# Optimization experiments

Hardware: AMD Instinct MI355X
Metric: run time of the kernel (lower is better)

## Reference

```python
import jax, jax.numpy as jnp
from jax import lax
import numpy as np

B, C, HH, WW = 8, 64, 128, 128
N = HH * WW
EPS = 1e-5


def _roll_h(xn, sign):
    # per-channel cyclic roll along H: out[b,c,h,w] = xn[b,c,(h - sign*c) % H, w]
    _, Cx, Hx, _ = xn.shape
    c = jnp.arange(Cx)[:, None]
    idx = (jnp.arange(Hx)[None, :] - sign * jnp.arange(Cx)[:, None]) % Hx  # (C,H)
    return xn[:, c, idx, :]


def _roll_w(xn, sign):
    return _roll_h(xn.transpose(0, 1, 3, 2), sign).transpose(0, 1, 3, 2)


def _ch_linear(xn, w, b):
    # nn.Linear over the channel dim of a BCHW tensor (token-MLP on (B,N,C))
    return jnp.einsum('bchw,cd->bdhw', xn, w) + b[None, :, None, None]


def _bn(xn, g, b):
    # BatchNorm2d, training-mode stats (biased var over B,H,W)
    m = xn.mean(axis=(0, 2, 3), keepdims=True)
    v = xn.var(axis=(0, 2, 3), keepdims=True)
    return (xn - m) * lax.rsqrt(v + EPS) * g[None, :, None, None] + b[None, :, None, None]


def _dwconv(xn, w, dil, pad):
    return lax.conv_general_dilated(xn, w, (1, 1), ((pad, pad), (pad, pad)),
                                    rhs_dilation=(dil, dil),
                                    dimension_numbers=('NCHW', 'OIHW', 'NCHW'),
                                    feature_group_count=xn.shape[1])


def _pc(xn, w):
    # 1x1 pointwise conv, no bias; w: (C_out, C_in)
    return jnp.einsum('bchw,oc->bohw', xn, w)


def lgff_forward(x, fc1_w, fc1_b, fc2_w, fc2_b, fc3_w, fc3_b, fc4_w, fc4_b,
                 fc5_w, fc5_b, ln_g, ln_b, pc_w, dw_w, dw_b, dw_bn_g, dw_bn_b,
                 dd_w, dd_bn_g, dd_bn_b, se_w1, se_b1, se_w2, se_b2, H, W):
    Bx, Nx, Cx = x.shape
    xn = x.transpose(0, 2, 1).reshape(Bx, Cx, H, W)
    # branch 1: roll+c along H -> fc1 -> GELU -> roll+c along W -> fc2
    a = jax.nn.gelu(_ch_linear(_roll_h(xn, 1), fc1_w, fc1_b), approximate=False)
    x_1 = _ch_linear(_roll_w(a, 1), fc2_w, fc2_b) + xn
    # branch 2: roll-c along W -> fc3 -> GELU -> roll+c along H -> fc4
    b = jax.nn.gelu(_ch_linear(_roll_w(xn, -1), fc3_w, fc3_b), approximate=False)
    x_2 = _ch_linear(_roll_h(b, 1), fc4_w, fc4_b) + xn
    # concat along feature dim (token layout dim=2 == channel dim here), LayerNorm(2C), fc5
    xc = jnp.concatenate([x_1, x_2], axis=1)  # (B, 2C, H, W)
    m = xc.mean(axis=1, keepdims=True)
    v = xc.var(axis=1, keepdims=True)
    xc = (xc - m) * lax.rsqrt(v + EPS) * ln_g[None, :, None, None] + ln_b[None, :, None, None]
    x1 = _ch_linear(xc, fc5_w, fc5_b) + xn
    # conv fusion part
    x2 = _pc(x1, pc_w)
    y = jax.nn.relu(_bn(_dwconv(x2, dw_w, 1, 1) + dw_b[None, :, None, None], dw_bn_g, dw_bn_b))
    y = jax.nn.relu(_bn(_dwconv(y, dd_w, 2, 2), dd_bn_g, dd_bn_b))
    y = _pc(y, pc_w)
    # four branches x3..x6 share identical weights/input -> identical outputs
    x7 = 4.0 * (x2 * y)
    # SE block
    s = x7.mean(axis=(2, 3), keepdims=True)  # (B,C,1,1)
    e = jax.nn.relu(jnp.einsum('bcij,oc->boij', s, se_w1) + se_b1[None, :, None, None])
    e = jax.nn.sigmoid(jnp.einsum('bcij,oc->boij', e, se_w2) + se_b2[None, :, None, None])
    return x7 + x7 * e  # (B, C, H, W)


def setup_inputs():
    key = jax.random.key(0)
    ks = jax.random.split(key, 12)
    r = C // 8
    inp = {
        'x': jax.random.normal(ks[0], (B, N, C), jnp.float32),
        'fc1_w': jax.random.normal(ks[1], (C, C), jnp.float32) * 0.02,
        'fc1_b': jnp.zeros((C,), jnp.float32),
        'fc2_w': jax.random.normal(ks[2], (C, C), jnp.float32) * 0.02,
        'fc2_b': jnp.zeros((C,), jnp.float32),
        'fc3_w': jax.random.normal(ks[3], (C, C), jnp.float32) * 0.02,
        'fc3_b': jnp.zeros((C,), jnp.float32),
        'fc4_w': jax.random.normal(ks[4], (C, C), jnp.float32) * 0.02,
        'fc4_b': jnp.zeros((C,), jnp.float32),
        'fc5_w': jax.random.normal(ks[5], (2 * C, C), jnp.float32) * 0.02,
        'fc5_b': jnp.zeros((C,), jnp.float32),
        'ln_g': jnp.ones((2 * C,), jnp.float32),
        'ln_b': jnp.zeros((2 * C,), jnp.float32),
        'pc_w': jax.random.normal(ks[6], (C, C), jnp.float32) * np.sqrt(2.0 / C).astype(np.float32),
        'dw_w': jax.random.normal(ks[7], (C, 1, 3, 3), jnp.float32) * np.sqrt(2.0 / 9.0).astype(np.float32),
        'dw_b': jnp.zeros((C,), jnp.float32),
        'dw_bn_g': jnp.ones((C,), jnp.float32),
        'dw_bn_b': jnp.zeros((C,), jnp.float32),
        'dd_w': jax.random.normal(ks[8], (C, 1, 3, 3), jnp.float32) * np.sqrt(2.0 / 9.0).astype(np.float32),
        'dd_bn_g': jnp.ones((C,), jnp.float32),
        'dd_bn_b': jnp.zeros((C,), jnp.float32),
        'se_w1': jax.random.normal(ks[9], (r, C), jnp.float32) * np.sqrt(2.0 / r).astype(np.float32),
        'se_b1': jnp.zeros((r,), jnp.float32),
        'se_w2': jax.random.normal(ks[10], (C, r), jnp.float32) * np.sqrt(2.0 / C).astype(np.float32),
        'se_b2': jnp.zeros((C,), jnp.float32),
        'H': HH,
        'W': WW,
    }
    return inp


def reference(x, fc1_w, fc1_b, fc2_w, fc2_b, fc3_w, fc3_b, fc4_w, fc4_b,
              fc5_w, fc5_b, ln_g, ln_b, pc_w, dw_w, dw_b, dw_bn_g, dw_bn_b,
              dd_w, dd_bn_g, dd_bn_b, se_w1, se_b1, se_w2, se_b2, H, W):
    return lgff_forward(x, fc1_w, fc1_b, fc2_w, fc2_b, fc3_w, fc3_b, fc4_w, fc4_b,
                        fc5_w, fc5_b, ln_g, ln_b, pc_w, dw_w, dw_b, dw_bn_g, dw_bn_b,
                        dd_w, dd_bn_g, dd_bn_b, se_w1, se_b1, se_w2, se_b2, H, W)
```

## Files before the change

### kernel.cpp

```cpp
#include <hip/hip_runtime.h>

constexpr int NB  = 8;
constexpr int NC  = 64;
constexpr int NH  = 128;
constexpr int NW  = 128;
constexpr int NHW = NH * NW;
constexpr int CHW = NC * NHW;
constexpr int SZ  = NB * CHW;
constexpr int NPOS = NB * NHW;
constexpr float EPS = 1e-5f;

typedef unsigned short u16;
using bf8   = __attribute__((ext_vector_type(8))) short;
using u16x8 = __attribute__((ext_vector_type(8))) u16;
using f32x4 = __attribute__((ext_vector_type(4))) float;

static __device__ inline short f2bf(float f) {
    union { float f; unsigned int u; } v; v.f = f;
    unsigned int r = v.u + 0x7fffu + ((v.u >> 16) & 1u);
    return (short)(r >> 16);
}
static __device__ inline float bf2f(u16 u) {
    union { unsigned int i; float f; } v; v.i = ((unsigned int)u) << 16;
    return v.f;
}

__global__ void k_transpose(const float* __restrict__ x, u16* __restrict__ xn) {
    __shared__ float t[64 * 65];
    int b   = blockIdx.x >> 8;
    int hw0 = (blockIdx.x & 255) << 6;
    int tid = threadIdx.x;
    #pragma unroll
    for (int k = 0; k < 16; ++k) {
        int idx = tid + (k << 8);
        int c = idx & 63, hwl = idx >> 6;
        t[c * 65 + hwl] = x[((size_t)b * NHW + hw0 + hwl) * NC + c];
    }
    __syncthreads();
    #pragma unroll
    for (int k = 0; k < 16; ++k) {
        int idx = tid + (k << 8);
        int hwl = idx & 63, c = idx >> 6;
        xn[(size_t)(b * NC + c) * NHW + hw0 + hwl] = (u16)f2bf(t[c * 65 + hwl]);
    }
}

__global__ void k_pq(const float* __restrict__ w5, const float* __restrict__ lng,
                     const float* __restrict__ lnb, float* __restrict__ PQ) {
    int d = threadIdx.x;
    float P = 0.f, Q = 0.f;
    for (int c = 0; c < 128; ++c) {
        float wv = w5[c * 64 + d];
        P += lng[c] * wv;
        Q += lnb[c] * wv;
    }
    PQ[d] = P; PQ[64 + d] = Q;
}

__global__ __launch_bounds__(256) void
k_mfc2s(const u16* __restrict__ xn,
        const float* __restrict__ w1, const float* __restrict__ b1,
        const float* __restrict__ w3, const float* __restrict__ b3,
        u16* __restrict__ t1, u16* __restrict__ t2) {
    __shared__ short wA[64 * 64];
    __shared__ short wB[64 * 64];
    __shared__ u16 tA[64 * 68];
    __shared__ u16 tB[64 * 132];
    int tid = threadIdx.x;
    int l = tid & 63, wv = tid >> 6;

    int p0 = blockIdx.x * 64;
    int b  = p0 >> 14;
    int hw0 = p0 & (NHW - 1);
    int h  = hw0 >> 7, w0 = hw0 & 127;
    const u16* inb = xn + (size_t)b * CHW;

    #pragma unroll
    for (int i = 0; i < 8; ++i) {
        int c0 = wv * 2 + i * 8;
        unsigned int pa = (unsigned int)(u16)f2bf(w1[c0 * 64 + l]) |
                          ((unsigned int)(u16)f2bf(w1[(c0 + 1) * 64 + l]) << 16);
        *(unsigned int*)&wA[l * 64 + (c0 ^ ((l & 7) << 3))] = pa;
        unsigned int pb = (unsigned int)(u16)f2bf(w3[c0 * 64 + l]) |
                          ((unsigned int)(u16)f2bf(w3[(c0 + 1) * 64 + l]) << 16);
        *(unsigned int*)&wB[l * 64 + (c0 ^ ((l & 7) << 3))] = pb;
    }
    #pragma unroll
    for (int k = 0; k < 2; ++k) {
        int i = tid + k * 256;
        int c = i >> 3, seg = i & 7;
        int gr = (h - c) & 127;
        *(u16x8*)&tA[c * 68 + seg * 8] = *(const u16x8*)(inb + c * NHW + gr * NW + w0 + seg * 8);
    }
    #pragma unroll
    for (int k = 0; k < 4; ++k) {
        int i = tid + k * 256;
        int c = i >> 4, seg = i & 15;
        *(u16x8*)&tB[c * 132 + seg * 8] = *(const u16x8*)(inb + c * NHW + h * NW + seg * 8);
    }
    __syncthreads();

    int q = l >> 4, col = l & 15;
    int pidx = wv * 16 + col;

    f32x4 acc1[4], acc2[4];
    #pragma unroll
    for (int dt = 0; dt < 4; ++dt) {
        acc1[dt] = (f32x4){0.f, 0.f, 0.f, 0.f};
        acc2[dt] = (f32x4){0.f, 0.f, 0.f, 0.f};
    }
    #pragma unroll
    for (int ks = 0; ks < 2; ++ks) {
        bf8 f1, f2;
        #pragma unroll
        for (int j = 0; j < 8; ++j) {
            int c = ks * 32 + q * 8 + j;
            f1[j] = (short)tA[c * 68 + pidx];
            f2[j] = (short)tB[c * 132 + ((w0 + pidx + c) & 127)];
        }
        #pragma unroll
        for (int dt = 0; dt < 4; ++dt) {
            int d = dt * 16 + col;
            int wo = (ks * 32 + q * 8) ^ ((d & 7) << 3);
            acc1[dt] = __builtin_amdgcn_mfma_f32_16x16x32_bf16(*(bf8*)&wA[d * 64 + wo], f1, acc1[dt], 0, 0, 0);
            acc2[dt] = __builtin_amdgcn_mfma_f32_16x16x32_bf16(*(bf8*)&wB[d * 64 + wo], f2, acc2[dt], 0, 0, 0);
        }
    }

    size_t obase = (size_t)b * CHW + hw0;
    #pragma unroll
    for (int dt = 0; dt < 4; ++dt) {
        #pragma unroll
        for (int r = 0; r < 4; ++r) {
            int d = dt * 16 + q * 4 + r;
            float v1 = acc1[dt][r] + b1[d];
            v1 = 0.5f * v1 * (1.f + erff(v1 * 0.70710678118654752f));
            float v2 = acc2[dt][r] + b3[d];
            v2 = 0.5f * v2 * (1.f + erff(v2 * 0.70710678118654752f));
            t1[obase + (size_t)d * NHW + pidx - pidx + ((wv * 16 + col))] = (u16)f2bf(v1);
            t2[obase + (size_t)d * NHW + ((wv * 16 + col))] = (u16)f2bf(v2);
        }
    }
}

__global__ __launch_bounds__(256) void
k_ffuse(const u16* __restrict__ t1, const u16* __restrict__ t2,
        const u16* __restrict__ xnb,
        const float* __restrict__ fc2w, const float* __restrict__ fc2b,
        const float* __restrict__ fc4w, const float* __restrict__ fc4b,
        const float* __restrict__ w5, const float* __restrict__ lng,
        const float* __restrict__ PQ, const float* __restrict__ b5,
        u16* __restrict__ x1out) {
    __shared__ short wA[64 * 64];
    __shared__ short wB[64 * 64];
    __shared__ short wG[64 * 128];
    __shared__ short xt[64 * 136];

    int tid = threadIdx.x;
    int l = tid & 63, wv = tid >> 6;

    #pragma unroll
    for (int i = 0; i < 8; ++i) {
        int c0 = wv * 2 + i * 8;
        unsigned int pa = (unsigned int)(u16)f2bf(fc2w[c0 * 64 + l]) |
                          ((unsigned int)(u16)f2bf(fc2w[(c0 + 1) * 64 + l]) << 16);
        *(unsigned int*)&wA[l * 64 + (c0 ^ ((l & 7) << 3))] = pa;
        unsigned int pb = (unsigned int)(u16)f2bf(fc4w[c0 * 64 + l]) |
                          ((unsigned int)(u16)f2bf(fc4w[(c0 + 1) * 64 + l]) << 16);
        *(unsigned int*)&wB[l * 64 + (c0 ^ ((l & 7) << 3))] = pb;
    }
    #pragma unroll
    for (int i = 0; i < 16; ++i) {
        int c0 = wv * 2 + i * 8;
        unsigned int pk = (unsigned int)(u16)f2bf(lng[c0] * w5[c0 * 64 + l]) |
                          ((unsigned int)(u16)f2bf(lng[c0 + 1] * w5[(c0 + 1) * 64 + l]) << 16);
        *(unsigned int*)&wG[l * 128 + (c0 ^ ((l & 7) << 3))] = pk;
    }
    __syncthreads();

    int q = l >> 4, col = l & 15;
    int p  = blockIdx.x * 64 + wv * 16 + col;
    int b  = p >> 14;
    int hw = p & (NHW - 1);
    int h  = hw >> 7, w = hw & 127;
    size_t base = (size_t)b * CHW;
    int pos = wv * 16 + col;

    f32x4 acc1[4], acc2[4];
    #pragma unroll
    for (int dt = 0; dt < 4; ++dt) {
        acc1[dt] = (f32x4){0.f, 0.f, 0.f, 0.f};
        acc2[dt] = (f32x4){0.f, 0.f, 0.f, 0.f};
    }
    #pragma unroll
    for (int ks = 0; ks < 2; ++ks) {
        bf8 f1, f2;
        #pragma unroll
        for (int j = 0; j < 8; ++j) {
            int c = ks * 32 + q * 8 + j;
            f1[j] = (short)t1[base + c * NHW + (h << 7) + ((w - c) & 127)];
            f2[j] = (short)t2[base + c * NHW + (((h - c) & 127) << 7) + w];
        }
        #pragma unroll
        for (int dt = 0; dt < 4; ++dt) {
            int d = dt * 16 + col;
            int wo = (ks * 32 + q * 8) ^ ((d & 7) << 3);
            acc1[dt] = __builtin_amdgcn_mfma_f32_16x16x32_bf16(*(bf8*)&wA[d * 64 + wo], f1, acc1[dt], 0, 0, 0);
            acc2[dt] = __builtin_amdgcn_mfma_f32_16x16x32_bf16(*(bf8*)&wB[d * 64 + wo], f2, acc2[dt], 0, 0, 0);
        }
    }

    float xr[16];
    #pragma unroll
    for (int dt = 0; dt < 4; ++dt)
        #pragma unroll
        for (int r = 0; r < 4; ++r)
            xr[dt * 4 + r] = bf2f(xnb[base + (size_t)(dt * 16 + q * 4 + r) * NHW + hw]);

    float s = 0.f, sq = 0.f;
    #pragma unroll
    for (int dt = 0; dt < 4; ++dt) {
        float v1[4], v2[4];
        #pragma unroll
        for (int r = 0; r < 4; ++r) {
            int d = dt * 16 + q * 4 + r;
            v1[r] = acc1[dt][r] + fc2b[d] + xr[dt * 4 + r];
            v2[r] = acc2[dt][r] + fc4b[d] + xr[dt * 4 + r];
            s += v1[r] + v2[r];
            sq += v1[r] * v1[r] + v2[r] * v2[r];
        }
        unsigned int pk0 = (unsigned int)(u16)f2bf(v1[0]) | ((unsigned int)(u16)f2bf(v1[1]) << 16);
        unsigned int pk1 = (unsigned int)(u16)f2bf(v1[2]) | ((unsigned int)(u16)f2bf(v1[3]) << 16);
        *(uint2*)&xt[pos * 136 + dt * 16 + q * 4] = make_uint2(pk0, pk1);
        unsigned int pk2 = (unsigned int)(u16)f2bf(v2[0]) | ((unsigned int)(u16)f2bf(v2[1]) << 16);
        unsigned int pk3 = (unsigned int)(u16)f2bf(v2[2]) | ((unsigned int)(u16)f2bf(v2[3]) << 16);
        *(uint2*)&xt[pos * 136 + 64 + dt * 16 + q * 4] = make_uint2(pk2, pk3);
    }
    s  += __shfl_xor(s, 16);  s += __shfl_xor(s, 32);
    sq += __shfl_xor(sq, 16); sq += __shfl_xor(sq, 32);
    float m    = s * (1.f / 128.f);
    float var  = sq * (1.f / 128.f) - m * m;
    float rstd = rsqrtf(var + EPS);
    float mr   = m * rstd;
    __syncthreads();

    f32x4 acc[4];
    #pragma unroll
    for (int dt = 0; dt < 4; ++dt) acc[dt] = (f32x4){0.f, 0.f, 0.f, 0.f};
    #pragma unroll
    for (int ks = 0; ks < 4; ++ks) {
        bf8 bfr = *(bf8*)&xt[pos * 136 + ks * 32 + q * 8];
        #pragma unroll
        for (int dt = 0; dt < 4; ++dt) {
            int d = dt * 16 + col;
            bf8 afr = *(bf8*)&wG[d * 128 + ((ks * 32 + q * 8) ^ ((d & 7) << 3))];
            acc[dt] = __builtin_amdgcn_mfma_f32_16x16x32_bf16(afr, bfr, acc[dt], 0, 0, 0);
        }
    }

    size_t obase = base + hw;
    #pragma unroll
    for (int dt = 0; dt < 4; ++dt) {
        #pragma unroll
        for (int r = 0; r < 4; ++r) {
            int d = dt * 16 + q * 4 + r;
            float val = rstd * acc[dt][r] + PQ[64 + d] - mr * PQ[d] + b5[d] + xr[dt * 4 + r];
            x1out[obase + (size_t)d * NHW] = (u16)f2bf(val);
        }
    }
}

template<bool BNRELU_IN>
__global__ __launch_bounds__(256) void
k_mfc(const u16* __restrict__ in, const float* __restrict__ wgt,
      const float* __restrict__ psum, const float* __restrict__ psq,
      const float* __restrict__ bng, const float* __restrict__ bnb,
      u16* __restrict__ out) {
    __shared__ short wt[64 * 64];
    __shared__ float scl[64], sft[64];
    int tid = threadIdx.x;
    int l = tid & 63, wv = tid >> 6;

    #pragma unroll
    for (int i = 0; i < 16; ++i) {
        int d = wv * 16 + i;
        wt[d * 64 + (l ^ ((d & 7) << 3))] = f2bf(wgt[d * 64 + l]);
    }
    if (BNRELU_IN && tid < 64) {
        float s = 0.f, qv = 0.f;
        #pragma unroll
        for (int i = 0; i < 32; ++i) {
            int bb = i >> 2, j = i & 3;
            int idx = ((bb * 64 + tid) << 2) + j;
            s += psum[idx]; qv += psq[idx];
        }
        const float inv = 1.f / (float)(NB * NHW);
        float m = s * inv;
        float var = qv * inv - m * m;
        float rs = rsqrtf(var + EPS);
        float sc = rs * bng[tid];
        scl[tid] = sc;
        sft[tid] = bnb[tid] - m * sc;
    }
    __syncthreads();

    int q = l >> 4, col = l & 15;
    int p  = blockIdx.x * 64 + wv * 16 + col;
    int b  = p >> 14;
    int hw = p & (NHW - 1);
    const u16* inb = in + (size_t)b * CHW;

    f32x4 acc[4];
    #pragma unroll
    for (int dt = 0; dt < 4; ++dt) acc[dt] = (f32x4){0.f, 0.f, 0.f, 0.f};

    #pragma unroll
    for (int ks = 0; ks < 2; ++ks) {
        bf8 bfr;
        #pragma unroll
        for (int j = 0; j < 8; ++j) {
            int c = ks * 32 + q * 8 + j;
            u16 raw = inb[c * NHW + hw];
            if (BNRELU_IN) {
                float v = fmaxf(bf2f(raw) * scl[c] + sft[c], 0.f);
                bfr[j] = f2bf(v);
            } else {
                bfr[j] = (short)raw;
            }
        }
        #pragma unroll
        for (int dt = 0; dt < 4; ++dt) {
            int d = dt * 16 + col;
            bf8 afr = *(bf8*)&wt[d * 64 + ((ks * 32 + q * 8) ^ ((d & 7) << 3))];
            acc[dt] = __builtin_amdgcn_mfma_f32_16x16x32_bf16(afr, bfr, acc[dt], 0, 0, 0);
        }
    }

    size_t obase = (size_t)b * CHW + hw;
    #pragma unroll
    for (int dt = 0; dt < 4; ++dt)
        #pragma unroll
        for (int r = 0; r < 4; ++r) {
            int d = dt * 16 + q * 4 + r;
            out[obase + (size_t)d * NHW] = (u16)f2bf(acc[dt][r]);
        }
}

template<int DIL, bool HASBIAS, bool BNIN>
__global__ __launch_bounds__(256) void
k_dwlds(const u16* __restrict__ in, const float* __restrict__ wgt,
        const float* __restrict__ bias,
        const float* __restrict__ psumIn, const float* __restrict__ psqIn,
        const float* __restrict__ bng, const float* __restrict__ bnb,
        u16* __restrict__ out, float* __restrict__ psumOut, float* __restrict__ psqOut) {
    constexpr int STR = 136;
    __shared__ float tile[36 * STR];
    __shared__ float ss[256], sq[256];

    int blk = ((blockIdx.x & 7) << 8) | (blockIdx.x >> 3);
    int q   = blk & 3;
    int bc  = blk >> 2;
    int c   = bc & 63;
    int r0  = q * 32;
    int tid = threadIdx.x;
    const u16* ip = in + (size_t)bc * NHW;

    float scale = 0.f, shift = 0.f;
    if (BNIN) {
        float s = 0.f, qv = 0.f;
        #pragma unroll
        for (int i = 0; i < 32; ++i) {
            int bb = i >> 2, j = i & 3;
            int idx = ((bb * 64 + c) << 2) + j;
            s += psumIn[idx]; qv += psqIn[idx];
        }
        const float inv = 1.f / (float)(NB * NHW);
        float m = s * inv;
        float var = qv * inv - m * m;
        float rs = rsqrtf(var + EPS);
        scale = rs * bng[c];
        shift = bnb[c] - m * scale;
    }

    #pragma unroll 1
    for (int idx = tid; idx < 36 * 16; idx += 256) {
        int lr = idx >> 4, u = idx & 15;
        int gr = r0 - 2 + lr;
        float v[8] = {0.f, 0.f, 0.f, 0.f, 0.f, 0.f, 0.f, 0.f};
        if (gr >= 0 && gr < NH) {
            u16x8 raw = *(const u16x8*)(ip + gr * NW + u * 8);
            #pragma unroll
            for (int j = 0; j < 8; ++j) {
                float f = bf2f(raw[j]);
                if (BNIN) f = fmaxf(f * scale + shift, 0.f);
                v[j] = f;
            }
        }
        *(float4*)&tile[lr * STR + 4 + u * 8]     = make_float4(v[0], v[1], v[2], v[3]);
        *(float4*)&tile[lr * STR + 4 + u * 8 + 4] = make_float4(v[4], v[5], v[6], v[7]);
        if (u == 0)  *(float4*)&tile[lr * STR]       = make_float4(0.f, 0.f, 0.f, 0.f);
        if (u == 15) *(float4*)&tile[lr * STR + 132] = make_float4(0.f, 0.f, 0.f, 0.f);
    }
    __syncthreads();

    float wc[9];
    #pragma unroll
    for (int k = 0; k < 9; ++k) wc[k] = wgt[c * 9 + k];

    int row  = tid >> 3;
    int col0 = (tid & 7) * 16;
    float o[16];
    float bb = HASBIAS ? bias[c] : 0.f;
    #pragma unroll
    for (int j = 0; j < 16; ++j) o[j] = bb;

    #pragma unroll
    for (int i = 0; i < 3; ++i) {
        const float* rp = &tile[(row + 2 + (i - 1) * DIL) * STR + 4 + col0];
        float4 A  = *(const float4*)(rp - 4);
        float4 B0 = *(const float4*)(rp);
        float4 B1 = *(const float4*)(rp + 4);
        float4 B2 = *(const float4*)(rp + 8);
        float4 B3 = *(const float4*)(rp + 12);
        float4 Cc = *(const float4*)(rp + 16);
        float ww[24] = {A.x,A.y,A.z,A.w, B0.x,B0.y,B0.z,B0.w, B1.x,B1.y,B1.z,B1.w,
                        B2.x,B2.y,B2.z,B2.w, B3.x,B3.y,B3.z,B3.w, Cc.x,Cc.y,Cc.z,Cc.w};
        float w0 = wc[3 * i], w1 = wc[3 * i + 1], w2 = wc[3 * i + 2];
        #pragma unroll
        for (int j = 0; j < 16; ++j)
            o[j] += w0 * ww[4 + j - DIL] + w1 * ww[4 + j] + w2 * ww[4 + j + DIL];
    }

    u16* op = out + (size_t)bc * NHW + (r0 + row) * NW + col0;
    u16x8 o1, o2;
    #pragma unroll
    for (int j = 0; j < 8; ++j) { o1[j] = (u16)f2bf(o[j]); o2[j] = (u16)f2bf(o[8 + j]); }
    *(u16x8*)(op)     = o1;
    *(u16x8*)(op + 8) = o2;

    float s = 0.f, qq = 0.f;
    #pragma unroll
    for (int j = 0; j < 16; ++j) { s += o[j]; qq += o[j] * o[j]; }
    ss[tid] = s; sq[tid] = qq; __syncthreads();
    for (int off = 128; off > 0; off >>= 1) {
        if (tid < off) { ss[tid] += ss[tid + off]; sq[tid] += sq[tid + off]; }
        __syncthreads();
    }
    if (tid == 0) { psumOut[blk] = ss[0]; psqOut[blk] = sq[0]; }
}

__global__ void k_se_reduce(const u16* __restrict__ x2, const u16* __restrict__ y3,
                            float* __restrict__ s4) {
    __shared__ float ss[256];
    int q   = blockIdx.x & 3;
    int bc  = blockIdx.x >> 2;
    int tid = threadIdx.x;
    const u16* a  = x2 + (size_t)bc * NHW + q * (NHW / 4);
    const u16* b_ = y3 + (size_t)bc * NHW + q * (NHW / 4);
    float acc = 0.f;
    #pragma unroll
    for (int i = 0; i < 2; ++i) {
        u16x8 av = *(const u16x8*)(a + (tid + i * 256) * 8);
        u16x8 bv = *(const u16x8*)(b_ + (tid + i * 256) * 8);
        #pragma unroll
        for (int j = 0; j < 8; ++j) acc += bf2f(av[j]) * bf2f(bv[j]);
    }
    ss[tid] = acc; __syncthreads();
    for (int o = 128; o > 0; o >>= 1) {
        if (tid < o) ss[tid] += ss[tid + o];
        __syncthreads();
    }
    if (tid == 0) s4[blockIdx.x] = ss[0];
}

__global__ void k_final8(const u16* __restrict__ x2, const u16* __restrict__ y3,
                         const float* __restrict__ s4,
                         const float* __restrict__ w1, const float* __restrict__ b1,
                         const float* __restrict__ w2, const float* __restrict__ b2,
                         float* __restrict__ out) {
    __shared__ float sh[64], e1[8], ev[1];
    int tid = threadIdx.x;
    int bc = blockIdx.x >> 3;
    int b  = bc >> 6, c = bc & 63;

    if (tid < 64) {
        float sv = 0.f;
        #pragma unroll
        for (int j = 0; j < 4; ++j) sv += s4[(b * 64 + tid) * 4 + j];
        sh[tid] = sv * (4.f / (float)NHW);
    }
    __syncthreads();
    if (tid < 8) {
        float a = b1[tid];
        for (int cc = 0; cc < 64; ++cc) a += sh[cc] * w1[tid * 64 + cc];
        e1[tid] = a > 0.f ? a : 0.f;
    }
    __syncthreads();
    if (tid == 0) {
        float a = b2[c];
        #pragma unroll
        for (int j = 0; j < 8; ++j) a += e1[j] * w2[c * 8 + j];
        ev[0] = 1.f / (1.f + expf(-a));
    }
    __syncthreads();

    int t = blockIdx.x * 256 + tid;
    float f = 4.f * (1.f + ev[0]);
    u16x8 av = *(const u16x8*)(x2 + (size_t)t * 8);
    u16x8 bv = *(const u16x8*)(y3 + (size_t)t * 8);
    float4 o0, o1;
    o0.x = f * bf2f(av[0]) * bf2f(bv[0]); o0.y = f * bf2f(av[1]) * bf2f(bv[1]);
    o0.z = f * bf2f(av[2]) * bf2f(bv[2]); o0.w = f * bf2f(av[3]) * bf2f(bv[3]);
    o1.x = f * bf2f(av[4]) * bf2f(bv[4]); o1.y = f * bf2f(av[5]) * bf2f(bv[5]);
    o1.z = f * bf2f(av[6]) * bf2f(bv[6]); o1.w = f * bf2f(av[7]) * bf2f(bv[7]);
    *(float4*)(out + (size_t)t * 8)     = o0;
    *(float4*)(out + (size_t)t * 8 + 4) = o1;
}

extern "C" void kernel_launch(void* const* d_in, const int* in_sizes, int n_in,
                              void* d_out, int out_size, void* d_ws, size_t ws_size,
                              hipStream_t stream) {
    const float* x     = (const float*)d_in[0];
    const float* fc1w  = (const float*)d_in[1];
    const float* fc1b  = (const float*)d_in[2];
    const float* fc2w  = (const float*)d_in[3];
    const float* fc2b  = (const float*)d_in[4];
    const float* fc3w  = (const float*)d_in[5];
    const float* fc3b  = (const float*)d_in[6];
    const float* fc4w  = (const float*)d_in[7];
    const float* fc4b  = (const float*)d_in[8];
    const float* fc5w  = (const float*)d_in[9];
    const float* fc5b  = (const float*)d_in[10];
    const float* lng   = (const float*)d_in[11];
    const float* lnb   = (const float*)d_in[12];
    const float* pcw   = (const float*)d_in[13];
    const float* dww   = (const float*)d_in[14];
    const float* dwb   = (const float*)d_in[15];
    const float* dwbng = (const float*)d_in[16];
    const float* dwbnb = (const float*)d_in[17];
    const float* ddw   = (const float*)d_in[18];
    const float* ddbng = (const float*)d_in[19];
    const float* ddbnb = (const float*)d_in[20];
    const float* sew1  = (const float*)d_in[21];
    const float* seb1  = (const float*)d_in[22];
    const float* sew2  = (const float*)d_in[23];
    const float* seb2  = (const float*)d_in[24];

    float* out = (float*)d_out;
    u16* wsu = (u16*)d_ws;
    u16* bufA = wsu;
    u16* bufB = wsu + (size_t)SZ;
    u16* bufC = wsu + (size_t)2 * SZ;
    u16* bufD = wsu + (size_t)3 * SZ;
    float* st = (float*)(wsu + (size_t)4 * SZ);
    float* psumA = st;
    float* psqA  = st + 2048;
    float* psumB = st + 4096;
    float* psqB  = st + 6144;
    float* svec  = st + 8192;
    float* pqv   = st + 10240;

    dim3 blk(256);
    const float* nil = nullptr;

    k_transpose<<<NB * (NHW / 64), blk, 0, stream>>>(x, bufA);
    k_pq<<<1, 64, 0, stream>>>(fc5w, lng, lnb, pqv);
    k_mfc2s<<<NPOS / 64, blk, 0, stream>>>(bufA, fc1w, fc1b, fc3w, fc3b, bufB, bufC);
    k_ffuse<<<NPOS / 64, blk, 0, stream>>>(bufB, bufC, bufA, fc2w, fc2b, fc4w, fc4b,
                                           fc5w, lng, pqv, fc5b, bufD);
    k_mfc<false><<<NPOS / 64, blk, 0, stream>>>(bufD, pcw, nil, nil, nil, nil, bufA);
    k_dwlds<1, true, false><<<2048, blk, 0, stream>>>(bufA, dww, dwb, nil, nil, nil, nil, bufB, psumA, psqA);
    k_dwlds<2, false, true><<<2048, blk, 0, stream>>>(bufB, ddw, nil, psumA, psqA, dwbng, dwbnb, bufC, psumB, psqB);
    k_mfc<true><<<NPOS / 64, blk, 0, stream>>>(bufC, pcw, psumB, psqB, ddbng, ddbnb, bufD);
    k_se_reduce<<<NB * NC * 4, blk, 0, stream>>>(bufA, bufD, svec);
    k_final8<<<SZ / 2048, blk, 0, stream>>>(bufA, bufD, svec, sew1, seb1, sew2, seb2, out);
}
```

Baseline: 154.3 us.

## Issue global activation loads before weight staging and vectorize MFMA output stores

The 1x1-conv MFMA kernels now issue their per-position activation gathers into registers at kernel start, before the weight-to-LDS staging and barrier, so global latency overlaps the weight setup. k_mfc2 also drops the LDS staging of the rolled input tiles and gathers the rolled inputs straight from global memory. MFMA operand order is swapped in k_mfc2 and k_mfc so each lane holds four consecutive positions for one output channel, which allows 8-byte vector stores instead of scalar 2-byte stores. The cost is higher register pressure, and the global gathers in k_mfc2 are less coalesced than the old LDS tiles.

```diff
diff --git a/kernel.cpp b/kernel.cpp
--- a/kernel.cpp
+++ b/kernel.cpp
@@ -13,6 +13,7 @@
 typedef unsigned short u16;
 using bf8   = __attribute__((ext_vector_type(8))) short;
 using u16x8 = __attribute__((ext_vector_type(8))) u16;
+using u16x4 = __attribute__((ext_vector_type(4))) u16;
 using f32x4 = __attribute__((ext_vector_type(4))) float;
 
 static __device__ inline short f2bf(float f) {
@@ -58,22 +59,31 @@
 }
 
 __global__ __launch_bounds__(256) void
-k_mfc2s(const u16* __restrict__ xn,
-        const float* __restrict__ w1, const float* __restrict__ b1,
-        const float* __restrict__ w3, const float* __restrict__ b3,
-        u16* __restrict__ t1, u16* __restrict__ t2) {
+k_mfc2(const u16* __restrict__ xn,
+       const float* __restrict__ w1, const float* __restrict__ b1,
+       const float* __restrict__ w3, const float* __restrict__ b3,
+       u16* __restrict__ t1, u16* __restrict__ t2) {
     __shared__ short wA[64 * 64];
     __shared__ short wB[64 * 64];
-    __shared__ u16 tA[64 * 68];
-    __shared__ u16 tB[64 * 132];
     int tid = threadIdx.x;
     int l = tid & 63, wv = tid >> 6;
-
-    int p0 = blockIdx.x * 64;
-    int b  = p0 >> 14;
-    int hw0 = p0 & (NHW - 1);
-    int h  = hw0 >> 7, w0 = hw0 & 127;
+    int q = l >> 4, col = l & 15;
+
+    int p  = blockIdx.x * 64 + wv * 16 + col;
+    int b  = p >> 14;
+    int hw = p & (NHW - 1);
+    int h  = hw >> 7, w = hw & 127;
     const u16* inb = xn + (size_t)b * CHW;
+
+    bf8 f1a[2], f2a[2];
+    #pragma unroll
+    for (int ks = 0; ks < 2; ++ks)
+        #pragma unroll
+        for (int j = 0; j < 8; ++j) {
+            int c = ks * 32 + q * 8 + j;
+            f1a[ks][j] = (short)inb[c * NHW + (((h - c) & 127) << 7) + w];
+            f2a[ks][j] = (short)inb[c * NHW + (h << 7) + ((w + c) & 127)];
+        }
 
     #pragma unroll
     for (int i = 0; i < 8; ++i) {
@@ -85,23 +95,7 @@
                           ((unsigned int)(u16)f2bf(w3[(c0 + 1) * 64 + l]) << 16);
         *(unsigned int*)&wB[l * 64 + (c0 ^ ((l & 7) << 3))] = pb;
     }
-    #pragma unroll
-    for (int k = 0; k < 2; ++k) {
-        int i = tid + k * 256;
-        int c = i >> 3, seg = i & 7;
-        int gr = (h - c) & 127;
-        *(u16x8*)&tA[c * 68 + seg * 8] = *(const u16x8*)(inb + c * NHW + gr * NW + w0 + seg * 8);
-    }
-    #pragma unroll
-    for (int k = 0; k < 4; ++k) {
-        int i = tid + k * 256;
-        int c = i >> 4, seg = i & 15;
-        *(u16x8*)&tB[c * 132 + seg * 8] = *(const u16x8*)(inb + c * NHW + h * NW + seg * 8);
-    }
-    __syncthreads();
-
-    int q = l >> 4, col = l & 15;
-    int pidx = wv * 16 + col;
+    __syncthreads();
 
     f32x4 acc1[4], acc2[4];
     #pragma unroll
@@ -111,35 +105,33 @@
     }
     #pragma unroll
     for (int ks = 0; ks < 2; ++ks) {
-        bf8 f1, f2;
-        #pragma unroll
-        for (int j = 0; j < 8; ++j) {
-            int c = ks * 32 + q * 8 + j;
-            f1[j] = (short)tA[c * 68 + pidx];
-            f2[j] = (short)tB[c * 132 + ((w0 + pidx + c) & 127)];
-        }
         #pragma unroll
         for (int dt = 0; dt < 4; ++dt) {
             int d = dt * 16 + col;
             int wo = (ks * 32 + q * 8) ^ ((d & 7) << 3);
-            acc1[dt] = __builtin_amdgcn_mfma_f32_16x16x32_bf16(*(bf8*)&wA[d * 64 + wo], f1, acc1[dt], 0, 0, 0);
-            acc2[dt] = __builtin_amdgcn_mfma_f32_16x16x32_bf16(*(bf8*)&wB[d * 64 + wo], f2, acc2[dt], 0, 0, 0);
-        }
-    }
-
-    size_t obase = (size_t)b * CHW + hw0;
+            acc1[dt] = __builtin_amdgcn_mfma_f32_16x16x32_bf16(f1a[ks], *(bf8*)&wA[d * 64 + wo], acc1[dt], 0, 0, 0);
+            acc2[dt] = __builtin_amdgcn_mfma_f32_16x16x32_bf16(f2a[ks], *(bf8*)&wB[d * 64 + wo], acc2[dt], 0, 0, 0);
+        }
+    }
+
+    int hwst = (blockIdx.x * 64 + wv * 16 + q * 4) & (NHW - 1);
+    size_t ob = (size_t)b * CHW + hwst;
     #pragma unroll
     for (int dt = 0; dt < 4; ++dt) {
+        int d = dt * 16 + col;
+        float bb1 = b1[d], bb3 = b3[d];
+        u16x4 o1v, o2v;
         #pragma unroll
         for (int r = 0; r < 4; ++r) {
-            int d = dt * 16 + q * 4 + r;
-            float v1 = acc1[dt][r] + b1[d];
+            float v1 = acc1[dt][r] + bb1;
             v1 = 0.5f * v1 * (1.f + erff(v1 * 0.70710678118654752f));
-            float v2 = acc2[dt][r] + b3[d];
+            float v2 = acc2[dt][r] + bb3;
             v2 = 0.5f * v2 * (1.f + erff(v2 * 0.70710678118654752f));
-            t1[obase + (size_t)d * NHW + pidx - pidx + ((wv * 16 + col))] = (u16)f2bf(v1);
-            t2[obase + (size_t)d * NHW + ((wv * 16 + col))] = (u16)f2bf(v2);
-        }
+            o1v[r] = (u16)f2bf(v1);
+            o2v[r] = (u16)f2bf(v2);
+        }
+        *(u16x4*)&t1[ob + (size_t)d * NHW] = o1v;
+        *(u16x4*)&t2[ob + (size_t)d * NHW] = o2v;
     }
 }
 
@@ -158,6 +150,30 @@
 
     int tid = threadIdx.x;
     int l = tid & 63, wv = tid >> 6;
+    int q = l >> 4, col = l & 15;
+
+    int p  = blockIdx.x * 64 + wv * 16 + col;
+    int b  = p >> 14;
+    int hw = p & (NHW - 1);
+    int h  = hw >> 7, w = hw & 127;
+    size_t base = (size_t)b * CHW;
+    int pos = wv * 16 + col;
+
+    bf8 f1a[2], f2a[2];
+    #pragma unroll
+    for (int ks = 0; ks < 2; ++ks)
+        #pragma unroll
+        for (int j = 0; j < 8; ++j) {
+            int c = ks * 32 + q * 8 + j;
+            f1a[ks][j] = (short)t1[base + c * NHW + (h << 7) + ((w - c) & 127)];
+            f2a[ks][j] = (short)t2[base + c * NHW + (((h - c) & 127) << 7) + w];
+        }
+    u16 xrr[16];
+    #pragma unroll
+    for (int dt = 0; dt < 4; ++dt)
+        #pragma unroll
+        for (int r = 0; r < 4; ++r)
+            xrr[dt * 4 + r] = xnb[base + (size_t)(dt * 16 + q * 4 + r) * NHW + hw];
 
     #pragma unroll
     for (int i = 0; i < 8; ++i) {
@@ -178,14 +194,6 @@
     }
     __syncthreads();
 
-    int q = l >> 4, col = l & 15;
-    int p  = blockIdx.x * 64 + wv * 16 + col;
-    int b  = p >> 14;
-    int hw = p & (NHW - 1);
-    int h  = hw >> 7, w = hw & 127;
-    size_t base = (size_t)b * CHW;
-    int pos = wv * 16 + col;
-
     f32x4 acc1[4], acc2[4];
     #pragma unroll
     for (int dt = 0; dt < 4; ++dt) {
@@ -194,28 +202,18 @@
     }
     #pragma unroll
     for (int ks = 0; ks < 2; ++ks) {
-        bf8 f1, f2;
-        #pragma unroll
-        for (int j = 0; j < 8; ++j) {
-            int c = ks * 32 + q * 8 + j;
-            f1[j] = (short)t1[base + c * NHW + (h << 7) + ((w - c) & 127)];
-            f2[j] = (short)t2[base + c * NHW + (((h - c) & 127) << 7) + w];
-        }
         #pragma unroll
         for (int dt = 0; dt < 4; ++dt) {
             int d = dt * 16 + col;
             int wo = (ks * 32 + q * 8) ^ ((d & 7) << 3);
-            acc1[dt] = __builtin_amdgcn_mfma_f32_16x16x32_bf16(*(bf8*)&wA[d * 64 + wo], f1, acc1[dt], 0, 0, 0);
-            acc2[dt] = __builtin_amdgcn_mfma_f32_16x16x32_bf16(*(bf8*)&wB[d * 64 + wo], f2, acc2[dt], 0, 0, 0);
+            acc1[dt] = __builtin_amdgcn_mfma_f32_16x16x32_bf16(*(bf8*)&wA[d * 64 + wo], f1a[ks], acc1[dt], 0, 0, 0);
+            acc2[dt] = __builtin_amdgcn_mfma_f32_16x16x32_bf16(*(bf8*)&wB[d * 64 + wo], f2a[ks], acc2[dt], 0, 0, 0);
         }
     }
 
     float xr[16];
     #pragma unroll
-    for (int dt = 0; dt < 4; ++dt)
-        #pragma unroll
-        for (int r = 0; r < 4; ++r)
-            xr[dt * 4 + r] = bf2f(xnb[base + (size_t)(dt * 16 + q * 4 + r) * NHW + hw]);
+    for (int i = 0; i < 16; ++i) xr[i] = bf2f(xrr[i]);
 
     float s = 0.f, sq = 0.f;
     #pragma unroll
@@ -280,6 +278,19 @@
     __shared__ float scl[64], sft[64];
     int tid = threadIdx.x;
     int l = tid & 63, wv = tid >> 6;
+    int q = l >> 4, col = l & 15;
+
+    int p  = blockIdx.x * 64 + wv * 16 + col;
+    int b  = p >> 14;
+    int hw = p & (NHW - 1);
+    const u16* inb = in + (size_t)b * CHW;
+
+    u16 raw[2][8];
+    #pragma unroll
+    for (int ks = 0; ks < 2; ++ks)
+        #pragma unroll
+        for (int j = 0; j < 8; ++j)
+            raw[ks][j] = inb[(ks * 32 + q * 8 + j) * NHW + hw];
 
     #pragma unroll
     for (int i = 0; i < 16; ++i) {
@@ -304,46 +315,43 @@
     }
     __syncthreads();
 
-    int q = l >> 4, col = l & 15;
-    int p  = blockIdx.x * 64 + wv * 16 + col;
-    int b  = p >> 14;
-    int hw = p & (NHW - 1);
-    const u16* inb = in + (size_t)b * CHW;
+    bf8 bfr[2];
+    #pragma unroll
+    for (int ks = 0; ks < 2; ++ks)
+        #pragma unroll
+        for (int j = 0; j < 8; ++j) {
+            if (BNRELU_IN) {
+                int c = ks * 32 + q * 8 + j;
+                float v = fmaxf(bf2f(raw[ks][j]) * scl[c] + sft[c], 0.f);
+                bfr[ks][j] = f2bf(v);
+            } else {
+                bfr[ks][j] = (short)raw[ks][j];
+            }
+        }
 
     f32x4 acc[4];
     #pragma unroll
     for (int dt = 0; dt < 4; ++dt) acc[dt] = (f32x4){0.f, 0.f, 0.f, 0.f};
-
     #pragma unroll
     for (int ks = 0; ks < 2; ++ks) {
-        bf8 bfr;
-        #pragma unroll
-        for (int j = 0; j < 8; ++j) {
-            int c = ks * 32 + q * 8 + j;
-            u16 raw = inb[c * NHW + hw];
-            if (BNRELU_IN) {
-                float v = fmaxf(bf2f(raw) * scl[c] + sft[c], 0.f);
-                bfr[j] = f2bf(v);
-            } else {
-                bfr[j] = (short)raw;
-            }
-        }
         #pragma unroll
         for (int dt = 0; dt < 4; ++dt) {
             int d = dt * 16 + col;
             bf8 afr = *(bf8*)&wt[d * 64 + ((ks * 32 + q * 8) ^ ((d & 7) << 3))];
-            acc[dt] = __builtin_amdgcn_mfma_f32_16x16x32_bf16(afr, bfr, acc[dt], 0, 0, 0);
-        }
-    }
-
-    size_t obase = (size_t)b * CHW + hw;
-    #pragma unroll
-    for (int dt = 0; dt < 4; ++dt)
-        #pragma unroll
-        for (int r = 0; r < 4; ++r) {
-            int d = dt * 16 + q * 4 + r;
-            out[obase + (size_t)d * NHW] = (u16)f2bf(acc[dt][r]);
-        }
+            acc[dt] = __builtin_amdgcn_mfma_f32_16x16x32_bf16(bfr[ks], afr, acc[dt], 0, 0, 0);
+        }
+    }
+
+    int hwst = (blockIdx.x * 64 + wv * 16 + q * 4) & (NHW - 1);
+    size_t ob = (size_t)b * CHW + hwst;
+    #pragma unroll
+    for (int dt = 0; dt < 4; ++dt) {
+        int d = dt * 16 + col;
+        u16x4 ov;
+        #pragma unroll
+        for (int r = 0; r < 4; ++r) ov[r] = (u16)f2bf(acc[dt][r]);
+        *(u16x4*)&out[ob + (size_t)d * NHW] = ov;
+    }
 }
 
 template<int DIL, bool HASBIAS, bool BNIN>
@@ -565,7 +573,7 @@
 
     k_transpose<<<NB * (NHW / 64), blk, 0, stream>>>(x, bufA);
     k_pq<<<1, 64, 0, stream>>>(fc5w, lng, lnb, pqv);
-    k_mfc2s<<<NPOS / 64, blk, 0, stream>>>(bufA, fc1w, fc1b, fc3w, fc3b, bufB, bufC);
+    k_mfc2<<<NPOS / 64, blk, 0, stream>>>(bufA, fc1w, fc1b, fc3w, fc3b, bufB, bufC);
     k_ffuse<<<NPOS / 64, blk, 0, stream>>>(bufB, bufC, bufA, fc2w, fc2b, fc4w, fc4b,
                                            fc5w, lng, pqv, fc5b, bufD);
     k_mfc<false><<<NPOS / 64, blk, 0, stream>>>(bufD, pcw, nil, nil, nil, nil, bufA);
```

New measurement: 178.9 us. 1.16x slower.
